# Kernel optimization log

Hardware: AMD Instinct MI355X
Metric: run time of the kernel (lower is better)

The kernel has to match this reference:

```python
import jax, jax.numpy as jnp
import numpy as np

# ---- problem constants (match init_kwargs) ----
M, N, DV = 4096, 8192, 4   # checks, variables, column weight
SEED = 0
MAX_ITER = 10
ALPHA = 0.8
CLAMP = 20.0
BATCH = 256
PAD_BIG = 1.0e6


def _build_code():
    """Deterministic regular-column-weight LDPC pcm + padded adjacency (mirrors torch __init__)."""
    rng = np.random.default_rng(SEED)
    pcm = np.zeros((M, N), dtype=np.uint8)
    for v in range(N):
        checks = rng.choice(M, size=DV, replace=False)
        pcm[checks, v] = 1
    check_indices, var_indices = np.nonzero(pcm)  # row-major: sorted by check
    num_edges = len(check_indices)
    check_adj_lists = [[] for _ in range(M)]
    var_adj_lists = [[] for _ in range(N)]
    for e in range(num_edges):
        check_adj_lists[int(check_indices[e])].append(e)
        var_adj_lists[int(var_indices[e])].append(e)
    max_dc = max(len(a) for a in check_adj_lists)
    max_dv = max(len(a) for a in var_adj_lists)
    check_adj = np.zeros((M, max_dc), dtype=np.int64)
    check_mask = np.zeros((M, max_dc), dtype=np.float32)
    for c, adj in enumerate(check_adj_lists):
        for j, e in enumerate(adj):
            check_adj[c, j] = e
            check_mask[c, j] = 1.0
    var_adj = np.zeros((N, max_dv), dtype=np.int64)
    var_mask = np.zeros((N, max_dv), dtype=np.float32)
    for v, adj in enumerate(var_adj_lists):
        for j, e in enumerate(adj):
            var_adj[v, j] = e
            var_mask[v, j] = 1.0
    return pcm, check_indices, var_indices, check_adj, check_mask, var_adj, var_mask


def setup_inputs() -> dict:
    key = jax.random.key(0)
    k1, k2 = jax.random.split(key)
    pcm, _, var_idx, check_adj, check_mask, var_adj, var_mask = _build_code()
    syndrome = jax.random.randint(k1, (BATCH, M), 0, 2).astype(jnp.float32)
    channel_llr = jax.random.normal(k2, (BATCH, N), dtype=jnp.float32) * 2.0
    return {
        "syndrome": syndrome,
        "channel_llr": channel_llr,
        "var_adj": jnp.asarray(var_adj, jnp.int32),
        "var_adj_mask": jnp.asarray(var_mask),
        "check_adj": jnp.asarray(check_adj, jnp.int32),
        "check_adj_mask": jnp.asarray(check_mask),
        "var_idx": jnp.asarray(var_idx, jnp.int32),
        "pcm_dense": jnp.asarray(pcm, jnp.float32),
    }


def reference(syndrome, channel_llr, var_adj, var_adj_mask, check_adj, check_adj_mask, var_idx, pcm_dense):
    B = syndrome.shape[0]
    E = var_idx.shape[0]
    s_sign = 1.0 - 2.0 * syndrome                      # [B, m]
    flat_cidx = check_adj.reshape(-1)                  # [m*max_dc]; padded slots point to edge 0 with value 0

    def step(ctv, _):
        # variable-node update: gather check->var messages per variable
        var_total = jnp.sum(ctv[:, var_adj] * var_adj_mask, axis=2)           # [B, n]
        vtc = channel_llr[:, var_idx] + var_total[:, var_idx] - ctv           # [B, E]
        vtc = jnp.clip(vtc, -CLAMP, CLAMP)
        # check-node min-sum update
        vg = vtc[:, check_adj]                                                # [B, m, dc]
        signs = jnp.where(vg >= 0.0, 1.0, -1.0)                               # sign(0) -> +1, as in torch path
        signs_m = signs * check_adj_mask + (1.0 - check_adj_mask)             # padded -> +1
        total_sign = s_sign[:, :, None] * jnp.prod(signs_m, axis=2, keepdims=True)
        excl_sign = total_sign * signs_m                                      # divide == multiply for +/-1
        absv = jnp.abs(vg) + (1.0 - check_adj_mask) * PAD_BIG                 # [B, m, dc]
        neg_top2, _ = jax.lax.top_k(-absv, 2)                                 # two smallest magnitudes
        min1 = -neg_top2[..., 0:1]
        min2 = -neg_top2[..., 1:2]
        is_min = jnp.abs(absv - min1) < 1e-9
        excl_min = jnp.where(is_min, min2, min1)
        ctv_new = ALPHA * excl_sign * excl_min * check_adj_mask               # [B, m, dc]
        # scatter back to flat edge layout (each real edge written exactly once; padded values are 0)
        ctv = jnp.zeros((B, E), ctv.dtype).at[:, flat_cidx].add(ctv_new.reshape(B, -1))
        return ctv, None

    ctv0 = jnp.zeros((B, E), jnp.float32)
    ctv, _ = jax.lax.scan(step, ctv0, None, length=MAX_ITER)

    var_total = jnp.sum(ctv[:, var_adj] * var_adj_mask, axis=2)
    total_llr = channel_llr + var_total
    marginals = jax.nn.sigmoid(-total_llr)                                    # [B, n]
    hard_decision = (marginals > 0.5).astype(jnp.int32)
    syn_hat = jnp.mod(jnp.round(hard_decision.astype(jnp.float32) @ pcm_dense.T), 2.0)
    converged = jnp.sum(jnp.abs(syn_hat - syndrome), axis=1) < 0.5
    return marginals, hard_decision, converged
```

## Files before the change

kernel.cpp:

```cpp
#include <hip/hip_runtime.h>
#include <math.h>


#define BLOCK 1024
#define NV    8192
#define MC    4096
#define NE    32768
#define VPT   (NV / BLOCK)
#define CPT   (MC / BLOCK)
#define NITER 10
#define ALPHA 0.8f
#define CLAMP 20.0f
#define MSGW  40896


__global__ __launch_bounds__(BLOCK)
void setup_sort(const float* __restrict__ check_mask,
                const int*   __restrict__ check_adj,
                int max_dc, int* __restrict__ ws)
{
    __shared__ int hist[64], base[64], wsum[16];
    __shared__ int sdeg[MC];
    const int t = threadIdx.x;
    if (t < 64) hist[t] = 0;
    __syncthreads();
    int deg[CPT];
#pragma unroll
    for (int k = 0; k < CPT; ++k) {
        const int c = t + k * BLOCK;
        int d = 0;
        for (int j = 0; j < max_dc; ++j)
            d += (check_mask[(size_t)c * max_dc + j] != 0.0f) ? 1 : 0;
        deg[k] = d;
        atomicAdd(&hist[d & 63], 1);
    }
    __syncthreads();
    if (t == 0) {
        int s = 0;
        for (int i = 0; i < 64; ++i) { base[i] = s; s += hist[i]; }
    }
    __syncthreads();
#pragma unroll
    for (int k = 0; k < CPT; ++k) {
        const int pos = atomicAdd(&base[deg[k] & 63], 1);
        sdeg[pos]    = deg[k];
        ws[MC + pos] = t + k * BLOCK;
    }
    __syncthreads();

    int psz[CPT];
    int s = 0;
#pragma unroll
    for (int k = 0; k < CPT; ++k) {
        const int d = sdeg[4 * t + k];
        psz[k] = s;
        s += d + 1 + (d & 1);
    }
    const int lane = t & 63, wv = t >> 6;
    int run = s;
#pragma unroll
    for (int off = 1; off < 64; off <<= 1) {
        const int n = __shfl_up(run, off, 64);
        if (lane >= off) run += n;
    }
    if (lane == 63) wsum[wv] = run;
    __syncthreads();
    if (t == 0) {
        int acc = 0;
        for (int w = 0; w < 16; ++w) { const int v = wsum[w]; wsum[w] = acc; acc += v; }
    }
    __syncthreads();
    const int tb = wsum[wv] + (run - s);
#pragma unroll
    for (int k = 0; k < CPT; ++k) {
        const int i = 4 * t + k;
        ws[i] = ((tb + psz[k]) & 0xFFFF) | (sdeg[i] << 16);
    }
}

template<int DMAX>
__device__ __forceinline__ void do_check(float* __restrict__ msg,
                                         int st, int d, float sgn, float pad)
{
    float x[DMAX];
    float min1 = pad, min2 = pad, prod = sgn;
#pragma unroll
    for (int j = 0; j < DMAX; ++j) {
        if (j >= d) break;
        x[j] = msg[st + j];
    }
#pragma unroll
    for (int j = 0; j < DMAX; ++j) {
        if (j >= d) break;
        prod = (x[j] < 0.0f) ? -prod : prod;
        const float a = fabsf(x[j]);
        min2 = __builtin_amdgcn_fmed3f(min1, min2, a);
        min1 = fminf(min1, a);
    }
    const float vm1 = ALPHA * min1;
    const float vm2 = ALPHA * min2;
#pragma unroll
    for (int j = 0; j < DMAX; ++j) {
        if (j >= d) break;
        const float m = (fabsf(fabsf(x[j]) - min1) < 1e-9f) ? vm2 : vm1;
        const float v = m * prod;
        msg[st + j] = (x[j] < 0.0f) ? -v : v;
    }
}

__device__ void do_check_big(float* __restrict__ msg,
                             int st, int d, float sgn, float pad)
{
    float min1 = pad, min2 = pad, prod = sgn;
    for (int j = 0; j < d; ++j) {
        const float xx = msg[st + j];
        prod = (xx < 0.0f) ? -prod : prod;
        const float a = fabsf(xx);
        min2 = __builtin_amdgcn_fmed3f(min1, min2, a);
        min1 = fminf(min1, a);
    }
    const float vm1 = ALPHA * min1;
    const float vm2 = ALPHA * min2;
    for (int j = 0; j < d; ++j) {
        const float xx = msg[st + j];
        const float m  = (fabsf(fabsf(xx) - min1) < 1e-9f) ? vm2 : vm1;
        const float v  = m * prod;
        msg[st + j] = (xx < 0.0f) ? -v : v;
    }
}

__global__ __launch_bounds__(BLOCK) __attribute__((amdgpu_waves_per_eu(4, 4)))
void bp_decode(const float* __restrict__ syndrome,
               const float* __restrict__ llr_g,
               const int*   __restrict__ var_adj,
               const int*   __restrict__ var_idx,
               const int*   __restrict__ check_adj,
               int max_dc,
               const int*   __restrict__ ws,
               float* __restrict__ out,
               int B)
{
    __shared__ float msg[MSGW];
    __shared__ float sh_e0;
    __shared__ int   mism;

    const int b = blockIdx.x;
    const int t = threadIdx.x;

    int cst[CPT], dsb[CPT];
    {
        int* posL = (int*)msg;
#pragma unroll
        for (int k = 0; k < CPT; ++k) {
            const int i = t + k * BLOCK;
            const int w = ws[i];
            const int c = ws[MC + i];
            const int pb = w & 0xFFFF;
            const int d  = w >> 16;
            cst[k] = pb;
            const int sb = (syndrome[(size_t)b * MC + c] > 0.5f) ? 1 : 0;
            dsb[k] = (d << 1) | sb;
            const int st = check_adj[(size_t)c * max_dc];
            for (int j = 0; j < d; ++j)
                posL[st + j] = pb + j;
        }
    }
    __syncthreads();

    const int  v0  = var_idx[0];
    const int4 r0  = ((const int4*)var_adj)[v0];
    const int  j0  = (r0.y == 0) ? 1 : (r0.z == 0) ? 2 : (r0.w == 0) ? 3 : 0;
    const bool own = (t == (v0 & (BLOCK - 1)));
    const int  k0  = v0 >> 10;

    int   vs[VPT][4];
    float llr[VPT];
    {
        const int* posL = (const int*)msg;
#pragma unroll
        for (int k = 0; k < VPT; ++k) {
            const int v = t + k * BLOCK;
            const int4 a = ((const int4*)var_adj)[v];
            vs[k][0] = posL[a.x]; vs[k][1] = posL[a.y];
            vs[k][2] = posL[a.z]; vs[k][3] = posL[a.w];
            llr[k] = llr_g[(size_t)b * NV + v];
        }
    }
    __syncthreads();

    for (int e = t; e < MSGW; e += BLOCK) msg[e] = 0.0f;
    __syncthreads();

    for (int it = 0; it < NITER; ++it) {
#pragma unroll
        for (int k = 0; k < VPT; ++k) {
            const float c0 = msg[vs[k][0]];
            const float c1 = msg[vs[k][1]];
            const float c2 = msg[vs[k][2]];
            const float c3 = msg[vs[k][3]];
            const float tot  = ((c0 + c1) + c2) + c3;
            const float bse  = llr[k] + tot;
            const float o0 = __builtin_amdgcn_fmed3f(bse - c0, -CLAMP, CLAMP);
            const float o1 = __builtin_amdgcn_fmed3f(bse - c1, -CLAMP, CLAMP);
            const float o2 = __builtin_amdgcn_fmed3f(bse - c2, -CLAMP, CLAMP);
            const float o3 = __builtin_amdgcn_fmed3f(bse - c3, -CLAMP, CLAMP);
            msg[vs[k][0]] = o0;
            msg[vs[k][1]] = o1;
            msg[vs[k][2]] = o2;
            msg[vs[k][3]] = o3;
            if (own && k == k0) {
                const float vv = (j0 == 0) ? o0 : (j0 == 1) ? o1
                               : (j0 == 2) ? o2 : o3;
                sh_e0 = fabsf(vv) + 1.0e6f;
            }
        }
        __syncthreads();
        const float pad = sh_e0;

#pragma unroll
        for (int k = 0; k < CPT; ++k) {
            const int   d   = dsb[k] >> 1;
            const float sgn = (dsb[k] & 1) ? -1.0f : 1.0f;
            const int   st  = cst[k];
            if (d <= 8)       do_check<8>(msg, st, d, sgn, pad);
            else if (d <= 12) do_check<12>(msg, st, d, sgn, pad);
            else if (d <= 16) do_check<16>(msg, st, d, sgn, pad);
            else              do_check_big(msg, st, d, sgn, pad);
        }
        __syncthreads();
    }

    float marg[VPT], hard[VPT];
#pragma unroll
    for (int k = 0; k < VPT; ++k) {
        const float c0 = msg[vs[k][0]];
        const float c1 = msg[vs[k][1]];
        const float c2 = msg[vs[k][2]];
        const float c3 = msg[vs[k][3]];
        const float tot = ((c0 + c1) + c2) + c3;
        const float tl  = llr[k] + tot;
        const float mg  = 1.0f / (1.0f + expf(tl));
        marg[k] = mg;
        hard[k] = (mg > 0.5f) ? 1.0f : 0.0f;
    }
    if (t == 0) mism = 0;
    __syncthreads();

    const size_t BN = (size_t)B * NV;
#pragma unroll
    for (int k = 0; k < VPT; ++k) {
        const int v = t + k * BLOCK;
        out[(size_t)b * NV + v]      = marg[k];
        out[BN + (size_t)b * NV + v] = hard[k];
        const float h = hard[k];
        msg[vs[k][0]] = h;
        msg[vs[k][1]] = h;
        msg[vs[k][2]] = h;
        msg[vs[k][3]] = h;
    }
    __syncthreads();

#pragma unroll
    for (int k = 0; k < CPT; ++k) {
        const int d  = dsb[k] >> 1;
        const int sb = dsb[k] & 1;
        const int st = cst[k];
        int par = 0;
        for (int j = 0; j < d; ++j)
            par ^= (msg[st + j] != 0.0f) ? 1 : 0;
        if (par != sb) mism = 1;
    }
    __syncthreads();
    if (t == 0) out[2 * BN + b] = mism ? 0.0f : 1.0f;
}

extern "C" void kernel_launch(void* const* d_in, const int* in_sizes, int n_in,
                              void* d_out, int out_size, void* d_ws, size_t ws_size,
                              hipStream_t stream) {
    const float* syndrome   = (const float*)d_in[0];
    const float* llr        = (const float*)d_in[1];
    const int*   var_adj    = (const int*)d_in[2];
    const int*   check_adj  = (const int*)d_in[4];
    const float* check_mask = (const float*)d_in[5];
    const int*   var_idx    = (const int*)d_in[6];
    float* out = (float*)d_out;
    int*   ws  = (int*)d_ws;

    const int B      = in_sizes[0] / MC;
    const int max_dc = in_sizes[4] / MC;

    setup_sort<<<1, BLOCK, 0, stream>>>(check_mask, check_adj, max_dc, ws);
    bp_decode<<<B, BLOCK, 0, stream>>>(syndrome, llr, var_adj, var_idx,
                                       check_adj, max_dc, ws, out, B);
}
```

Measured before the change: 367.6 us.

## Fold check-degree sort setup kernel into the decode kernel per block

Removes the single-block setup_sort launch and has every decode block recompute check degrees, the degree-sorted order and the padded offsets in shared memory. Degree counting switches to wave-wide ballot/popcount over the mask row instead of a per-thread serial loop. The aim is to drop a serialized one-block kernel and its launch gap, in exchange for redundant setup work and extra global reads of check_mask in each of the 256 blocks.

```diff
diff --git a/kernel.cpp b/kernel.cpp
--- a/kernel.cpp
+++ b/kernel.cpp
@@ -13,70 +13,7 @@
 #define CLAMP 20.0f
 #define MSGW  40896
 
-
-__global__ __launch_bounds__(BLOCK)
-void setup_sort(const float* __restrict__ check_mask,
-                const int*   __restrict__ check_adj,
-                int max_dc, int* __restrict__ ws)
-{
-    __shared__ int hist[64], base[64], wsum[16];
-    __shared__ int sdeg[MC];
-    const int t = threadIdx.x;
-    if (t < 64) hist[t] = 0;
-    __syncthreads();
-    int deg[CPT];
-#pragma unroll
-    for (int k = 0; k < CPT; ++k) {
-        const int c = t + k * BLOCK;
-        int d = 0;
-        for (int j = 0; j < max_dc; ++j)
-            d += (check_mask[(size_t)c * max_dc + j] != 0.0f) ? 1 : 0;
-        deg[k] = d;
-        atomicAdd(&hist[d & 63], 1);
-    }
-    __syncthreads();
-    if (t == 0) {
-        int s = 0;
-        for (int i = 0; i < 64; ++i) { base[i] = s; s += hist[i]; }
-    }
-    __syncthreads();
-#pragma unroll
-    for (int k = 0; k < CPT; ++k) {
-        const int pos = atomicAdd(&base[deg[k] & 63], 1);
-        sdeg[pos]    = deg[k];
-        ws[MC + pos] = t + k * BLOCK;
-    }
-    __syncthreads();
-
-    int psz[CPT];
-    int s = 0;
-#pragma unroll
-    for (int k = 0; k < CPT; ++k) {
-        const int d = sdeg[4 * t + k];
-        psz[k] = s;
-        s += d + 1 + (d & 1);
-    }
-    const int lane = t & 63, wv = t >> 6;
-    int run = s;
-#pragma unroll
-    for (int off = 1; off < 64; off <<= 1) {
-        const int n = __shfl_up(run, off, 64);
-        if (lane >= off) run += n;
-    }
-    if (lane == 63) wsum[wv] = run;
-    __syncthreads();
-    if (t == 0) {
-        int acc = 0;
-        for (int w = 0; w < 16; ++w) { const int v = wsum[w]; wsum[w] = acc; acc += v; }
-    }
-    __syncthreads();
-    const int tb = wsum[wv] + (run - s);
-#pragma unroll
-    for (int k = 0; k < CPT; ++k) {
-        const int i = 4 * t + k;
-        ws[i] = ((tb + psz[k]) & 0xFFFF) | (sdeg[i] << 16);
-    }
-}
+__device__ __forceinline__ int pad_stride(int d) { return d + 1 + (d & 1); }
 
 template<int DMAX>
 __device__ __forceinline__ void do_check(float* __restrict__ msg,
@@ -135,8 +72,8 @@
                const int*   __restrict__ var_adj,
                const int*   __restrict__ var_idx,
                const int*   __restrict__ check_adj,
+               const float* __restrict__ check_mask,
                int max_dc,
-               const int*   __restrict__ ws,
                float* __restrict__ out,
                int B)
 {
@@ -146,21 +83,100 @@
 
     const int b = blockIdx.x;
     const int t = threadIdx.x;
-
-    int cst[CPT], dsb[CPT];
+    const int lane = t & 63, wv = t >> 6;
+
+    int* arena = (int*)msg;
+    int* degR  = arena;
+    int* sSort = arena + MC;
+    int* rec1  = arena + 2 * MC;
+    int* rec2  = arena + 3 * MC;
+    int* hist  = arena + 4 * MC;
+    int* wsum  = arena + 4 * MC + 64;
+
+    if (t < 64) hist[t] = 0;
+    __syncthreads();
+
+    for (int c = wv; c < MC; c += 16) {
+        int d = 0;
+        for (int j0 = 0; j0 < max_dc; j0 += 64) {
+            const int j = j0 + lane;
+            const float m = (j < max_dc) ? check_mask[(size_t)c * max_dc + j] : 0.0f;
+            d += (int)__popcll(__ballot(m != 0.0f));
+        }
+        if (lane == 0) { degR[c] = d; atomicAdd(&hist[d & 63], 1); }
+    }
+    __syncthreads();
+
+    if (t == 0) {
+        int s = 0;
+        for (int i = 0; i < 64; ++i) { const int v = hist[i]; hist[i] = s; s += v; }
+    }
+    __syncthreads();
+
+#pragma unroll
+    for (int k = 0; k < CPT; ++k) {
+        const int c = t + k * BLOCK;
+        const int d = degR[c];
+        const int p = atomicAdd(&hist[d & 63], 1);
+        sSort[p] = (d & 63) | (c << 6);
+    }
+    __syncthreads();
+
     {
-        int* posL = (int*)msg;
+        int psz[CPT], pd[CPT], pc[CPT];
+        int s = 0;
 #pragma unroll
         for (int k = 0; k < CPT; ++k) {
-            const int i = t + k * BLOCK;
-            const int w = ws[i];
-            const int c = ws[MC + i];
-            const int pb = w & 0xFFFF;
-            const int d  = w >> 16;
-            cst[k] = pb;
-            const int sb = (syndrome[(size_t)b * MC + c] > 0.5f) ? 1 : 0;
-            dsb[k] = (d << 1) | sb;
-            const int st = check_adj[(size_t)c * max_dc];
+            const int w = sSort[4 * t + k];
+            const int d = w & 63;
+            pd[k] = d; pc[k] = w >> 6;
+            psz[k] = s;
+            s += pad_stride(d);
+        }
+        int run = s;
+#pragma unroll
+        for (int off = 1; off < 64; off <<= 1) {
+            const int n = __shfl_up(run, off, 64);
+            if (lane >= off) run += n;
+        }
+        if (lane == 63) wsum[wv] = run;
+        __syncthreads();
+        if (t == 0) {
+            int acc = 0;
+            for (int w = 0; w < 16; ++w) { const int v = wsum[w]; wsum[w] = acc; acc += v; }
+        }
+        __syncthreads();
+        const int tb = wsum[wv] + (run - s);
+#pragma unroll
+        for (int k = 0; k < CPT; ++k) {
+            const int i = 4 * t + k;
+            rec1[i] = ((tb + psz[k]) & 0xFFFF) | (pd[k] << 16);
+            rec2[i] = pc[k];
+        }
+    }
+    __syncthreads();
+
+    int cst[CPT], dsb[CPT], stE[CPT];
+#pragma unroll
+    for (int k = 0; k < CPT; ++k) {
+        const int i = t + k * BLOCK;
+        const int w = rec1[i];
+        const int c = rec2[i];
+        cst[k] = w & 0xFFFF;
+        const int d  = w >> 16;
+        const int sb = (syndrome[(size_t)b * MC + c] > 0.5f) ? 1 : 0;
+        dsb[k] = (d << 1) | sb;
+        stE[k] = check_adj[(size_t)c * max_dc];
+    }
+    __syncthreads();
+
+    {
+        int* posL = arena;
+#pragma unroll
+        for (int k = 0; k < CPT; ++k) {
+            const int d  = dsb[k] >> 1;
+            const int pb = cst[k];
+            const int st = stE[k];
             for (int j = 0; j < d; ++j)
                 posL[st + j] = pb + j;
         }
@@ -176,7 +192,7 @@
     int   vs[VPT][4];
     float llr[VPT];
     {
-        const int* posL = (const int*)msg;
+        const int* posL = arena;
 #pragma unroll
         for (int k = 0; k < VPT; ++k) {
             const int v = t + k * BLOCK;
@@ -284,12 +300,11 @@
     const float* check_mask = (const float*)d_in[5];
     const int*   var_idx    = (const int*)d_in[6];
     float* out = (float*)d_out;
-    int*   ws  = (int*)d_ws;
+    (void)d_ws; (void)ws_size;
 
     const int B      = in_sizes[0] / MC;
     const int max_dc = in_sizes[4] / MC;
 
-    setup_sort<<<1, BLOCK, 0, stream>>>(check_mask, check_adj, max_dc, ws);
     bp_decode<<<B, BLOCK, 0, stream>>>(syndrome, llr, var_adj, var_idx,
-                                       check_adj, max_dc, ws, out, B);
+                                       check_adj, check_mask, max_dc, out, B);
 }
```

Measured after the change: 483.7 us. 1.32x slower.
